# Optimization experiments

Measured on AMD Instinct MI355X. Metric: run time of the kernel, lower is better.

The kernel has to match this reference:

```python
import jax, jax.numpy as jnp
import numpy as np

NUM_HEADS = 16
THETA = 10000.0

def _apply_rope(x, positions):
    # x: [B, H, S, dh] with interleaved pairs; positions: [B, S] int
    dh = x.shape[-1]
    inv_freq = THETA ** (-jnp.arange(0, dh, 2, dtype=jnp.float32) / dh)  # [dh/2]
    ang = positions.astype(jnp.float32)[:, None, :, None] * inv_freq  # [B,1,S,dh/2]
    cos, sin = jnp.cos(ang), jnp.sin(ang)
    x1, x2 = x[..., 0::2], x[..., 1::2]
    out_even = x1 * cos - x2 * sin
    out_odd = x1 * sin + x2 * cos
    return jnp.stack([out_even, out_odd], axis=-1).reshape(x.shape)

def setup_inputs() -> dict:
    B, S, D = 2, 2048, 2048
    key = jax.random.key(0)
    ks = jax.random.split(key, 5)
    scale = 0.02
    inp = {
        'in_features': jax.random.normal(ks[0], (B, S, D), dtype=jnp.float32),
        'token_positions': jnp.broadcast_to(jnp.arange(S, dtype=jnp.int32), (B, S)),
        'mask': jnp.tril(jnp.ones((S, S), dtype=bool)),
        'q_proj_weight': jax.random.normal(ks[1], (D, D), dtype=jnp.float32) * scale,
        'k_proj_weight': jax.random.normal(ks[2], (D, D), dtype=jnp.float32) * scale,
        'v_proj_weight': jax.random.normal(ks[3], (D, D), dtype=jnp.float32) * scale,
        'o_proj_weight': jax.random.normal(ks[4], (D, D), dtype=jnp.float32) * scale,
    }
    return inp

def reference(in_features, token_positions, mask, q_proj_weight, k_proj_weight, v_proj_weight, o_proj_weight):
    B, S, d_in = in_features.shape
    d_k = q_proj_weight.shape[0]
    d_v = v_proj_weight.shape[0]
    H = NUM_HEADS
    dk_head, dv_head = d_k // H, d_v // H
    Q = jnp.einsum('bsd,kd->bsk', in_features, q_proj_weight).reshape(B, S, H, dk_head).transpose(0, 2, 1, 3)
    K = jnp.einsum('bsd,kd->bsk', in_features, k_proj_weight).reshape(B, S, H, dk_head).transpose(0, 2, 1, 3)
    V = jnp.einsum('bsd,vd->bsv', in_features, v_proj_weight).reshape(B, S, H, dv_head).transpose(0, 2, 1, 3)
    Q = _apply_rope(Q, token_positions)
    K = _apply_rope(K, token_positions)
    scores = jnp.einsum('bhqd,bhkd->bhqk', Q, K) / jnp.sqrt(jnp.float32(dk_head))
    scores = jnp.where(mask[None, None, :, :], scores, jnp.finfo(scores.dtype).min)
    attn = jax.nn.softmax(scores, axis=-1)
    out = jnp.einsum('bhqk,bhkd->bhqd', attn, V)  # [B,H,S,dv_head]
    out = out.transpose(0, 2, 1, 3).reshape(B, S, d_v)
    return jnp.einsum('bsv,mv->bsm', out, o_proj_weight)
```

## Files before the change

kernel.cpp:

```cpp
#include <hip/hip_runtime.h>
#include <hip/hip_bf16.h>
#include <cstdint>

typedef __bf16 bf16_t;
typedef __bf16 bf16x8 __attribute__((ext_vector_type(8)));
typedef __bf16 bf16x4 __attribute__((ext_vector_type(4)));
typedef float  f32x4  __attribute__((ext_vector_type(4)));

#define B_  2
#define S_  2048
#define D_  2048
#define H_  16
#define DH_ 128
#define LDQ 6144

__device__ __forceinline__ void gload_lds16(const bf16_t* g, bf16_t* l) {
    __builtin_amdgcn_global_load_lds(
        (const __attribute__((address_space(1))) void*)g,
        (__attribute__((address_space(3))) void*)l, 16, 0, 0);
}

#define BAR  do { asm volatile("" ::: "memory"); __builtin_amdgcn_s_barrier(); \
                  asm volatile("" ::: "memory"); } while (0)
#define WAITLGKM do { asm volatile("s_waitcnt lgkmcnt(0)" ::: "memory"); \
                      __builtin_amdgcn_sched_barrier(0); } while (0)

__global__ __launch_bounds__(256)
void cast_all_k(const float* __restrict__ X,  const float* __restrict__ Wq,
                const float* __restrict__ Wk, const float* __restrict__ Wv,
                const float* __restrict__ Wo,
                bf16_t* __restrict__ Xb, bf16_t* __restrict__ Wqkv,
                bf16_t* __restrict__ Wob) {
    long bid = blockIdx.x;
    const float* src; bf16_t* dst; long off;
    if      (bid <  8192) { src = X;  dst = Xb;             off = bid;         }
    else if (bid < 12288) { src = Wq; dst = Wqkv;           off = bid - 8192;  }
    else if (bid < 16384) { src = Wk; dst = Wqkv + 4194304; off = bid - 12288; }
    else if (bid < 20480) { src = Wv; dst = Wqkv + 8388608; off = bid - 16384; }
    else                  { src = Wo; dst = Wob;            off = bid - 20480; }
    long i = (off * 256 + threadIdx.x) * 4;
    float4 v = *(const float4*)(src + i);
    bf16x4 o = {(bf16_t)v.x, (bf16_t)v.y, (bf16_t)v.z, (bf16_t)v.w};
    *(bf16x4*)(dst + i) = o;
}

#define LDS8(s, row, chunk) \
    (*(const bf16x8*)((s) + (row) * 64 + ((((chunk) ^ ((row) & 7))) << 3)))

template<bool C_BF16, int BM, int BN, int WMG, int WNG>
__global__ __launch_bounds__(512, 1)
void gemm_nt9(const bf16_t* __restrict__ A, int lda,
              const bf16_t* __restrict__ B, int ldb,
              void* __restrict__ Cp, int ldc, int K, int nbx) {
    constexpr int WTM = BM / WMG;
    constexpr int MR  = WTM / 16;
    constexpr int NR  = 4;
    constexpr int MH  = MR / 2;
    constexpr int NH  = 2;
    constexpr int LA  = BM / 128;
    constexpr int LB  = BN / 128;
    __shared__ bf16_t sA[2][BM * 64];
    __shared__ bf16_t sB[2][BN * 64];

    const int tid  = threadIdx.x;
    const int w    = tid >> 6;
    const int lane = tid & 63;
    const int fr   = lane & 15;
    const int hi   = lane >> 4;
    const int wm   = w / WNG;
    const int wn   = w % WNG;

    const int nwg = gridDim.x;
    const int lin = blockIdx.x;
    const int swz = (lin & 7) * (nwg >> 3) + (lin >> 3);
    const long bm = (long)(swz / nbx) * BM;
    const long bn = (long)(swz % nbx) * BN;

    const int srow = tid >> 3;
    const int scol = ((tid & 7) ^ (srow & 7)) * 8;
    const bf16_t* Agp = A + (bm + srow) * (long)lda + scol;
    const bf16_t* Bgp = B + (bn + srow) * (long)ldb + scol;

#define STAGE_A(bsel, h, kt) { _Pragma("unroll") \
    for (int p = 0; p < LA; ++p) \
        gload_lds16(Agp + (long)((h) * (BM / 2) + p * 64) * lda + ((long)(kt) << 6), \
                    &sA[bsel][((h) * (BM / 2) + p * 64) * 64 + w * 512]); }
#define STAGE_B(bsel, h, kt) { _Pragma("unroll") \
    for (int p = 0; p < LB; ++p) \
        gload_lds16(Bgp + (long)((h) * (BN / 2) + p * 64) * ldb + ((long)(kt) << 6), \
                    &sB[bsel][((h) * (BN / 2) + p * 64) * 64 + w * 512]); }

    f32x4 acc[MR][NR] = {};
    const int nkt = K >> 6;

    STAGE_A(0, 0, 0) STAGE_A(0, 1, 0)
    STAGE_B(0, 0, 0) STAGE_B(0, 1, 0)
    if (nkt > 1) STAGE_A(1, 0, 1)
    asm volatile("s_waitcnt vmcnt(2)" ::: "memory");
    BAR;

    for (int t = 0; t < nkt; ++t) {
        const int c = t & 1;
        const bf16_t* sAc = sA[c];
        const bf16_t* sBc = sB[c];
        const bool st1 = t + 1 < nkt;
        const bool st2 = t + 2 < nkt;
        bf16x8 af[MH][2], ag[MH][2], bf0[NH][2], bf1[NH][2];

#pragma unroll
        for (int mi = 0; mi < MH; ++mi)
#pragma unroll
            for (int ks = 0; ks < 2; ++ks)
                af[mi][ks] = LDS8(sAc, wm * WTM + mi * 16 + fr, ks * 4 + hi);
#pragma unroll
        for (int ni = 0; ni < NH; ++ni)
#pragma unroll
            for (int ks = 0; ks < 2; ++ks)
                bf0[ni][ks] = LDS8(sBc, wn * 64 + ni * 16 + fr, ks * 4 + hi);
        if (st1) STAGE_A(c ^ 1, 1, t + 1)
        BAR; WAITLGKM;
        __builtin_amdgcn_s_setprio(1);
#pragma unroll
        for (int mi = 0; mi < MH; ++mi)
#pragma unroll
            for (int ni = 0; ni < NH; ++ni)
#pragma unroll
                for (int ks = 0; ks < 2; ++ks)
                    acc[mi][ni] = __builtin_amdgcn_mfma_f32_16x16x32_bf16(
                        af[mi][ks], bf0[ni][ks], acc[mi][ni], 0, 0, 0);
        __builtin_amdgcn_s_setprio(0);
        BAR;

#pragma unroll
        for (int ni = 0; ni < NH; ++ni)
#pragma unroll
            for (int ks = 0; ks < 2; ++ks)
                bf1[ni][ks] = LDS8(sBc, wn * 64 + 32 + ni * 16 + fr, ks * 4 + hi);
        if (st1) STAGE_B(c ^ 1, 0, t + 1)
        BAR; WAITLGKM;
        __builtin_amdgcn_s_setprio(1);
#pragma unroll
        for (int mi = 0; mi < MH; ++mi)
#pragma unroll
            for (int ni = 0; ni < NH; ++ni)
#pragma unroll
                for (int ks = 0; ks < 2; ++ks)
                    acc[mi][NH + ni] = __builtin_amdgcn_mfma_f32_16x16x32_bf16(
                        af[mi][ks], bf1[ni][ks], acc[mi][NH + ni], 0, 0, 0);
        __builtin_amdgcn_s_setprio(0);
        BAR;

#pragma unroll
        for (int mi = 0; mi < MH; ++mi)
#pragma unroll
            for (int ks = 0; ks < 2; ++ks)
                ag[mi][ks] = LDS8(sAc, wm * WTM + (MH + mi) * 16 + fr, ks * 4 + hi);
        if (st1) STAGE_B(c ^ 1, 1, t + 1)
        BAR; WAITLGKM;
        __builtin_amdgcn_s_setprio(1);
#pragma unroll
        for (int mi = 0; mi < MH; ++mi)
#pragma unroll
            for (int ni = 0; ni < NH; ++ni)
#pragma unroll
                for (int ks = 0; ks < 2; ++ks)
                    acc[MH + mi][ni] = __builtin_amdgcn_mfma_f32_16x16x32_bf16(
                        ag[mi][ks], bf0[ni][ks], acc[MH + mi][ni], 0, 0, 0);
        __builtin_amdgcn_s_setprio(0);
        BAR;

        if (st2) STAGE_A(c, 0, t + 2)
        __builtin_amdgcn_s_setprio(1);
#pragma unroll
        for (int mi = 0; mi < MH; ++mi)
#pragma unroll
            for (int ni = 0; ni < NH; ++ni)
#pragma unroll
                for (int ks = 0; ks < 2; ++ks)
                    acc[MH + mi][NH + ni] = __builtin_amdgcn_mfma_f32_16x16x32_bf16(
                        ag[mi][ks], bf1[ni][ks], acc[MH + mi][NH + ni], 0, 0, 0);
        __builtin_amdgcn_s_setprio(0);
        asm volatile("s_waitcnt vmcnt(2)" ::: "memory");
        BAR;
    }

#pragma unroll
    for (int m = 0; m < MR; ++m) {
        long r0 = bm + wm * WTM + m * 16 + hi * 4;
#pragma unroll
        for (int n = 0; n < NR; ++n) {
            long cc = bn + wn * 64 + n * 16 + fr;
#pragma unroll
            for (int v = 0; v < 4; ++v) {
                if (C_BF16)
                    ((bf16_t*)Cp)[(r0 + v) * (long)ldc + cc] = (bf16_t)acc[m][n][v];
                else
                    ((float*)Cp)[(r0 + v) * (long)ldc + cc] = acc[m][n][v];
            }
        }
    }
#undef STAGE_A
#undef STAGE_B
}

__global__ __launch_bounds__(256)
void rope_qk_k(bf16_t* __restrict__ QKV, const int* __restrict__ pos) {
    int t = blockIdx.x * 256 + threadIdx.x;
    int g = t & 15;
    int h = (t >> 4) & 15;
    int s = (t >> 8) & 2047;
    int b = t >> 19;
    long qa = ((long)(b * S_ + s)) * LDQ + h * DH_ + g * 8;
    long ka = qa + D_;
    float p = (float)pos[b * S_ + s];
    bf16x8 q = *(bf16x8*)(QKV + qa);
    bf16x8 k = *(bf16x8*)(QKV + ka);
#pragma unroll
    for (int e = 0; e < 4; ++e) {
        int i = g * 4 + e;
        float invf = exp2f(-(float)i * 0.20762050593045702f);
        float ang = p * invf;
        float sn, cs;
        __sincosf(ang, &sn, &cs);
        float q1 = (float)q[2 * e], q2 = (float)q[2 * e + 1];
        q[2 * e]     = (bf16_t)(q1 * cs - q2 * sn);
        q[2 * e + 1] = (bf16_t)(q1 * sn + q2 * cs);
        float k1 = (float)k[2 * e], k2 = (float)k[2 * e + 1];
        k[2 * e]     = (bf16_t)(k1 * cs - k2 * sn);
        k[2 * e + 1] = (bf16_t)(k1 * sn + k2 * cs);
    }
    *(bf16x8*)(QKV + qa) = q;
    *(bf16x8*)(QKV + ka) = k;
}

__global__ __launch_bounds__(256)
void transpose_v_k(const bf16_t* __restrict__ QKV, bf16_t* __restrict__ Vt) {
    __shared__ bf16_t tile[64][80];
    int t = threadIdx.x;
    int bh = blockIdx.z;
    int b = bh >> 4, h = bh & 15;
    long s0 = (long)blockIdx.x * 64;
    int d0 = blockIdx.y * 64;
    const bf16_t* src = QKV + ((long)b * S_ + s0) * LDQ + 2 * D_ + h * DH_ + d0;
#pragma unroll
    for (int p = 0; p < 2; ++p) {
        int r = (t >> 3) + p * 32;
        int c = (t & 7) * 8;
        *(bf16x8*)&tile[r][c] = *(const bf16x8*)&src[(long)r * LDQ + c];
    }
    __syncthreads();
    bf16_t* dst = Vt + ((long)bh * DH_ + d0) * S_ + s0;
#pragma unroll
    for (int p = 0; p < 2; ++p) {
        int d = (t >> 3) + p * 32;
        int c = (t & 7) * 8;
        bf16x8 v;
#pragma unroll
        for (int e = 0; e < 8; ++e) v[e] = tile[c + e][d];
        *(bf16x8*)&dst[(long)d * S_ + c] = v;
    }
}

__device__ __forceinline__ bf16x8 ldsw(const bf16_t* p, int row, int ecol) {
    return *(const bf16x8*)(p + row * 128 + (ecol ^ ((row & 7) << 3)));
}

__global__ __launch_bounds__(512, 1)
void flash_attn_k(const bf16_t* __restrict__ QKV, const bf16_t* __restrict__ Vt,
                  bf16_t* __restrict__ O) {
    __shared__ bf16_t Ksh[2][128 * 128];
    __shared__ bf16_t Vsh[2][128 * 128];
    __shared__ bf16_t Psh[128 * 128];

    const int tid  = threadIdx.x;
    const int w    = tid >> 6;
    const int lane = tid & 63;
    const int fr   = lane & 15;
    const int hi   = lane >> 4;
    const int hi8  = hi * 8;
    const int hi4  = hi * 4;
    const int w16  = w * 16;

    const int bid = blockIdx.x;
    const int qi  = 15 - (bid >> 5);
    const int bh  = bid & 31;
    const int b   = bh >> 4;
    const int h   = bh & 15;
    const long bS   = (long)b * S_;
    const int  qoff = h * DH_;
    const int  koff = D_ + h * DH_;
    const long vbase = (long)bh * DH_;

#pragma unroll
    for (int p = 0; p < 4; ++p) {
        int idx = p * 512 + tid;
        int row = idx >> 4;
        int sl  = (idx & 15) ^ (row & 7);
        gload_lds16(QKV + (bS + qi * 128 + row) * (long)LDQ + qoff + sl * 8,
                    &Psh[(p * 512 + w * 64) * 8]);
    }
#pragma unroll
    for (int p = 0; p < 4; ++p) {
        int idx = p * 512 + tid;
        int row = idx >> 4;
        int sl  = (idx & 15) ^ (row & 7);
        gload_lds16(QKV + (bS + row) * (long)LDQ + koff + sl * 8,
                    &Ksh[0][(p * 512 + w * 64) * 8]);
        gload_lds16(Vt + (vbase + row) * S_ + sl * 8,
                    &Vsh[0][(p * 512 + w * 64) * 8]);
    }
    asm volatile("s_waitcnt vmcnt(8)" ::: "memory");
    __builtin_amdgcn_s_barrier();
    asm volatile("" ::: "memory");

    bf16x8 qfrag[4];
#pragma unroll
    for (int kk = 0; kk < 4; ++kk)
        qfrag[kk] = ldsw(Psh, w16 + fr, kk * 32 + hi8);

    f32x4 o[8] = {};
    float m_run[4] = {-3.0e38f, -3.0e38f, -3.0e38f, -3.0e38f};
    float l_run[4] = {};

    const float SC = 0.08838834764831845f * 1.4426950408889634f;

    for (int kt = 0; kt <= qi; ++kt) {
        const int buf = kt & 1;
        if (kt < qi) {
#pragma unroll
            for (int p = 0; p < 4; ++p) {
                int idx = p * 512 + tid;
                int row = idx >> 4;
                int sl  = (idx & 15) ^ (row & 7);
                gload_lds16(QKV + (bS + (kt + 1) * 128 + row) * (long)LDQ + koff + sl * 8,
                            &Ksh[buf ^ 1][(p * 512 + w * 64) * 8]);
                gload_lds16(Vt + (vbase + row) * S_ + (kt + 1) * 128 + sl * 8,
                            &Vsh[buf ^ 1][(p * 512 + w * 64) * 8]);
            }
            asm volatile("s_waitcnt vmcnt(8)" ::: "memory");
        } else {
            asm volatile("s_waitcnt vmcnt(0)" ::: "memory");
        }
        __builtin_amdgcn_s_barrier();
        asm volatile("" ::: "memory");

        f32x4 sc[8];
#pragma unroll
        for (int j = 0; j < 8; ++j) {
            f32x4 z = {};
#pragma unroll
            for (int kk = 0; kk < 4; ++kk)
                z = __builtin_amdgcn_mfma_f32_16x16x32_bf16(
                        qfrag[kk], ldsw(Ksh[buf], j * 16 + fr, kk * 32 + hi8), z, 0, 0, 0);
            sc[j] = z;
        }

        const bool diag = (kt == qi);
#pragma unroll
        for (int j = 0; j < 8; ++j)
#pragma unroll
            for (int v = 0; v < 4; ++v) {
                float x = sc[j][v] * SC;
                if (diag && (j * 16 + fr > w16 + hi4 + v)) x = -3.0e38f;
                sc[j][v] = x;
            }

        float fsc[4];
#pragma unroll
        for (int v = 0; v < 4; ++v) {
            float m = fmaxf(fmaxf(fmaxf(sc[0][v], sc[1][v]), fmaxf(sc[2][v], sc[3][v])),
                            fmaxf(fmaxf(sc[4][v], sc[5][v]), fmaxf(sc[6][v], sc[7][v])));
            m = fmaxf(m, __shfl_xor(m, 1));
            m = fmaxf(m, __shfl_xor(m, 2));
            m = fmaxf(m, __shfl_xor(m, 4));
            m = fmaxf(m, __shfl_xor(m, 8));
            float mn = fmaxf(m_run[v], m);
            fsc[v] = exp2f(m_run[v] - mn);
            m_run[v] = mn;
            l_run[v] *= fsc[v];
        }
#pragma unroll
        for (int j2 = 0; j2 < 8; ++j2)
#pragma unroll
            for (int v = 0; v < 4; ++v) o[j2][v] *= fsc[v];

#pragma unroll
        for (int j = 0; j < 8; ++j)
#pragma unroll
            for (int v = 0; v < 4; ++v) {
                float p = exp2f(sc[j][v] - m_run[v]);
                l_run[v] += p;
                int row = w16 + hi4 + v;
                int col = j * 16 + fr;
                Psh[row * 128 + (col ^ ((row & 7) << 3))] = (bf16_t)p;
            }

        asm volatile("s_waitcnt lgkmcnt(0)" ::: "memory");
        __builtin_amdgcn_sched_barrier(0);

        bf16x8 pa[4];
#pragma unroll
        for (int kk = 0; kk < 4; ++kk)
            pa[kk] = ldsw(Psh, w16 + fr, kk * 32 + hi8);
#pragma unroll
        for (int j2 = 0; j2 < 8; ++j2)
#pragma unroll
            for (int kk = 0; kk < 4; ++kk)
                o[j2] = __builtin_amdgcn_mfma_f32_16x16x32_bf16(
                            pa[kk], ldsw(Vsh[buf], j2 * 16 + fr, kk * 32 + hi8), o[j2], 0, 0, 0);

        asm volatile("" ::: "memory");
        __builtin_amdgcn_s_barrier();
        asm volatile("" ::: "memory");
    }

#pragma unroll
    for (int v = 0; v < 4; ++v) {
        float l = l_run[v];
        l += __shfl_xor(l, 1);
        l += __shfl_xor(l, 2);
        l += __shfl_xor(l, 4);
        l += __shfl_xor(l, 8);
        l_run[v] = 1.0f / l;
    }
    const long orow = bS + qi * 128 + w16 + hi4;
#pragma unroll
    for (int j2 = 0; j2 < 8; ++j2)
#pragma unroll
        for (int v = 0; v < 4; ++v)
            O[(orow + v) * D_ + qoff + j2 * 16 + fr] = (bf16_t)(o[j2][v] * l_run[v]);
}

extern "C" void kernel_launch(void* const* d_in, const int* in_sizes, int n_in,
                              void* d_out, int out_size, void* d_ws, size_t ws_size,
                              hipStream_t stream) {
    const float* in_features = (const float*)d_in[0];
    const int*   positions   = (const int*)d_in[1];
    const float* Wq = (const float*)d_in[3];
    const float* Wk = (const float*)d_in[4];
    const float* Wv = (const float*)d_in[5];
    const float* Wo = (const float*)d_in[6];
    float* out = (float*)d_out;

    const size_t SZ_X   = (size_t)B_ * S_ * D_ * 2;
    const size_t SZ_W   = (size_t)D_ * D_ * 2;
    const size_t SZ_QKV = (size_t)B_ * S_ * LDQ * 2;
    if (ws_size < SZ_X * 3 + SZ_W * 4 + SZ_QKV) return;

    char* w = (char*)d_ws;
    bf16_t* Xb      = (bf16_t*)w;   w += SZ_X;
    bf16_t* Wqkv    = (bf16_t*)w;   w += SZ_W * 3;
    bf16_t* Wob     = (bf16_t*)w;   w += SZ_W;
    bf16_t* QKV     = (bf16_t*)w;   w += SZ_QKV;
    bf16_t* Vt      = (bf16_t*)w;   w += SZ_X;
    bf16_t* AttnOut = (bf16_t*)w;   w += SZ_X;

    cast_all_k<<<24576, 256, 0, stream>>>(in_features, Wq, Wk, Wv, Wo, Xb, Wqkv, Wob);

    gemm_nt9<true, 256, 256, 2, 4><<<384, 512, 0, stream>>>(Xb, D_, Wqkv, D_,
                                                            QKV, LDQ, D_, 24);

    rope_qk_k<<<4096, 256, 0, stream>>>(QKV, positions);
    transpose_v_k<<<dim3(32, 2, 32), 256, 0, stream>>>(QKV, Vt);

    flash_attn_k<<<512, 512, 0, stream>>>(QKV, Vt, AttnOut);

    gemm_nt9<false, 256, 128, 4, 2><<<256, 512, 0, stream>>>(AttnOut, D_, Wob, D_,
                                                             out, D_, D_, 16);
}
```

Baseline: 407.7 us.

## Generalize GEMM warp tiling and retile QKV projection to 256x192 blocks

Generalizes the GEMM template so per-warp N fragments and B-tile staging chunks derive from BN and the warp grid, allowing non-power-of-two tiles like 256x192. The QKV projection switches from 256x256 tiles with a 2x4 warp layout (384 blocks) to 256x192 tiles with a 4x2 layout (512 blocks), aiming for better CU balance across the 256 CUs. It also drops the explicit lgkmcnt(0) waits and sched barriers after each barrier, leaving LDS read waits to the compiler, and drains vmcnt fully on the final iterations. Removing the explicit waits changes how LDS reads overlap with MFMAs, and the odd tile shape changes register pressure and staging balance.

Result: no change. 401.4 us (-1.5%).

```diff
diff --git a/kernel.cpp b/kernel.cpp
--- a/kernel.cpp
+++ b/kernel.cpp
@@ -22,8 +22,6 @@
 
 #define BAR  do { asm volatile("" ::: "memory"); __builtin_amdgcn_s_barrier(); \
                   asm volatile("" ::: "memory"); } while (0)
-#define WAITLGKM do { asm volatile("s_waitcnt lgkmcnt(0)" ::: "memory"); \
-                      __builtin_amdgcn_sched_barrier(0); } while (0)
 
 __global__ __launch_bounds__(256)
 void cast_all_k(const float* __restrict__ X,  const float* __restrict__ Wq,
@@ -52,13 +50,16 @@
 void gemm_nt9(const bf16_t* __restrict__ A, int lda,
               const bf16_t* __restrict__ B, int ldb,
               void* __restrict__ Cp, int ldc, int K, int nbx) {
-    constexpr int WTM = BM / WMG;
-    constexpr int MR  = WTM / 16;
-    constexpr int NR  = 4;
-    constexpr int MH  = MR / 2;
-    constexpr int NH  = 2;
-    constexpr int LA  = BM / 128;
-    constexpr int LB  = BN / 128;
+    constexpr int MR   = BM / WMG / 16;
+    constexpr int NR   = BN / WNG / 16;
+    constexpr int MH   = MR / 2;
+    constexpr int M2   = MR - MH;
+    constexpr int N0   = NR / 2;
+    constexpr int N1   = NR - N0;
+    constexpr int NCB  = BN / 64;
+    constexpr int NCB1 = (NCB + 1) / 2;
+    constexpr int WTM  = MR * 16;
+    constexpr int WTN  = NR * 16;
     __shared__ bf16_t sA[2][BM * 64];
     __shared__ bf16_t sB[2][BN * 64];
 
@@ -82,20 +83,20 @@
     const bf16_t* Bgp = B + (bn + srow) * (long)ldb + scol;
 
 #define STAGE_A(bsel, h, kt) { _Pragma("unroll") \
-    for (int p = 0; p < LA; ++p) \
+    for (int p = 0; p < 2; ++p) \
         gload_lds16(Agp + (long)((h) * (BM / 2) + p * 64) * lda + ((long)(kt) << 6), \
                     &sA[bsel][((h) * (BM / 2) + p * 64) * 64 + w * 512]); }
-#define STAGE_B(bsel, h, kt) { _Pragma("unroll") \
-    for (int p = 0; p < LB; ++p) \
-        gload_lds16(Bgp + (long)((h) * (BN / 2) + p * 64) * ldb + ((long)(kt) << 6), \
-                    &sB[bsel][((h) * (BN / 2) + p * 64) * 64 + w * 512]); }
+#define STAGE_B(bsel, c0, c1, kt) { _Pragma("unroll") \
+    for (int p = (c0); p < (c1); ++p) \
+        gload_lds16(Bgp + (long)(p * 64) * ldb + ((long)(kt) << 6), \
+                    &sB[bsel][(p * 64) * 64 + w * 512]); }
 
     f32x4 acc[MR][NR] = {};
     const int nkt = K >> 6;
 
     STAGE_A(0, 0, 0) STAGE_A(0, 1, 0)
-    STAGE_B(0, 0, 0) STAGE_B(0, 1, 0)
-    if (nkt > 1) STAGE_A(1, 0, 1)
+    STAGE_B(0, 0, NCB, 0)
+    STAGE_A(1, 0, 1)
     asm volatile("s_waitcnt vmcnt(2)" ::: "memory");
     BAR;
 
@@ -105,7 +106,7 @@
         const bf16_t* sBc = sB[c];
         const bool st1 = t + 1 < nkt;
         const bool st2 = t + 2 < nkt;
-        bf16x8 af[MH][2], ag[MH][2], bf0[NH][2], bf1[NH][2];
+        bf16x8 af[MH][2], ag[M2][2], bf0[N0][2], bf1[N1][2];
 
 #pragma unroll
         for (int mi = 0; mi < MH; ++mi)
@@ -113,17 +114,17 @@
             for (int ks = 0; ks < 2; ++ks)
                 af[mi][ks] = LDS8(sAc, wm * WTM + mi * 16 + fr, ks * 4 + hi);
 #pragma unroll
-        for (int ni = 0; ni < NH; ++ni)
+        for (int ni = 0; ni < N0; ++ni)
 #pragma unroll
             for (int ks = 0; ks < 2; ++ks)
-                bf0[ni][ks] = LDS8(sBc, wn * 64 + ni * 16 + fr, ks * 4 + hi);
+                bf0[ni][ks] = LDS8(sBc, wn * WTN + ni * 16 + fr, ks * 4 + hi);
         if (st1) STAGE_A(c ^ 1, 1, t + 1)
-        BAR; WAITLGKM;
+        BAR;
         __builtin_amdgcn_s_setprio(1);
 #pragma unroll
         for (int mi = 0; mi < MH; ++mi)
 #pragma unroll
-            for (int ni = 0; ni < NH; ++ni)
+            for (int ni = 0; ni < N0; ++ni)
 #pragma unroll
                 for (int ks = 0; ks < 2; ++ks)
                     acc[mi][ni] = __builtin_amdgcn_mfma_f32_16x16x32_bf16(
@@ -132,36 +133,36 @@
         BAR;
 
 #pragma unroll
-        for (int ni = 0; ni < NH; ++ni)
+        for (int ni = 0; ni < N1; ++ni)
 #pragma unroll
             for (int ks = 0; ks < 2; ++ks)
-                bf1[ni][ks] = LDS8(sBc, wn * 64 + 32 + ni * 16 + fr, ks * 4 + hi);
-        if (st1) STAGE_B(c ^ 1, 0, t + 1)
-        BAR; WAITLGKM;
+                bf1[ni][ks] = LDS8(sBc, wn * WTN + (N0 + ni) * 16 + fr, ks * 4 + hi);
+        if (st1) STAGE_B(c ^ 1, 0, NCB1, t + 1)
+        BAR;
         __builtin_amdgcn_s_setprio(1);
 #pragma unroll
         for (int mi = 0; mi < MH; ++mi)
 #pragma unroll
-            for (int ni = 0; ni < NH; ++ni)
+            for (int ni = 0; ni < N1; ++ni)
 #pragma unroll
                 for (int ks = 0; ks < 2; ++ks)
-                    acc[mi][NH + ni] = __builtin_amdgcn_mfma_f32_16x16x32_bf16(
-                        af[mi][ks], bf1[ni][ks], acc[mi][NH + ni], 0, 0, 0);
+                    acc[mi][N0 + ni] = __builtin_amdgcn_mfma_f32_16x16x32_bf16(
+                        af[mi][ks], bf1[ni][ks], acc[mi][N0 + ni], 0, 0, 0);
         __builtin_amdgcn_s_setprio(0);
         BAR;
 
 #pragma unroll
-        for (int mi = 0; mi < MH; ++mi)
+        for (int mi = 0; mi < M2; ++mi)
 #pragma unroll
             for (int ks = 0; ks < 2; ++ks)
                 ag[mi][ks] = LDS8(sAc, wm * WTM + (MH + mi) * 16 + fr, ks * 4 + hi);
-        if (st1) STAGE_B(c ^ 1, 1, t + 1)
-        BAR; WAITLGKM;
+        if (st1) STAGE_B(c ^ 1, NCB1, NCB, t + 1)
+        BAR;
         __builtin_amdgcn_s_setprio(1);
 #pragma unroll
-        for (int mi = 0; mi < MH; ++mi)
-#pragma unroll
-            for (int ni = 0; ni < NH; ++ni)
+        for (int mi = 0; mi < M2; ++mi)
+#pragma unroll
+            for (int ni = 0; ni < N0; ++ni)
 #pragma unroll
                 for (int ks = 0; ks < 2; ++ks)
                     acc[MH + mi][ni] = __builtin_amdgcn_mfma_f32_16x16x32_bf16(
@@ -172,15 +173,16 @@
         if (st2) STAGE_A(c, 0, t + 2)
         __builtin_amdgcn_s_setprio(1);
 #pragma unroll
-        for (int mi = 0; mi < MH; ++mi)
-#pragma unroll
-            for (int ni = 0; ni < NH; ++ni)
+        for (int mi = 0; mi < M2; ++mi)
+#pragma unroll
+            for (int ni = 0; ni < N1; ++ni)
 #pragma unroll
                 for (int ks = 0; ks < 2; ++ks)
-                    acc[MH + mi][NH + ni] = __builtin_amdgcn_mfma_f32_16x16x32_bf16(
-                        ag[mi][ks], bf1[ni][ks], acc[MH + mi][NH + ni], 0, 0, 0);
+                    acc[MH + mi][N0 + ni] = __builtin_amdgcn_mfma_f32_16x16x32_bf16(
+                        ag[mi][ks], bf1[ni][ks], acc[MH + mi][N0 + ni], 0, 0, 0);
         __builtin_amdgcn_s_setprio(0);
-        asm volatile("s_waitcnt vmcnt(2)" ::: "memory");
+        if (st2) { asm volatile("s_waitcnt vmcnt(2)" ::: "memory"); }
+        else     { asm volatile("s_waitcnt vmcnt(0)" ::: "memory"); }
         BAR;
     }
 
@@ -189,7 +191,7 @@
         long r0 = bm + wm * WTM + m * 16 + hi * 4;
 #pragma unroll
         for (int n = 0; n < NR; ++n) {
-            long cc = bn + wn * 64 + n * 16 + fr;
+            long cc = bn + wn * WTN + n * 16 + fr;
 #pragma unroll
             for (int v = 0; v < 4; ++v) {
                 if (C_BF16)
@@ -457,8 +459,8 @@
 
     cast_all_k<<<24576, 256, 0, stream>>>(in_features, Wq, Wk, Wv, Wo, Xb, Wqkv, Wob);
 
-    gemm_nt9<true, 256, 256, 2, 4><<<384, 512, 0, stream>>>(Xb, D_, Wqkv, D_,
-                                                            QKV, LDQ, D_, 24);
+    gemm_nt9<true, 256, 192, 4, 2><<<512, 512, 0, stream>>>(Xb, D_, Wqkv, D_,
+                                                            QKV, LDQ, D_, 32);
 
     rope_qk_k<<<4096, 256, 0, stream>>>(QKV, positions);
     transpose_v_k<<<dim3(32, 2, 32), 256, 0, stream>>>(QKV, Vt);
```
